# Performance work log

Hardware: AMD Instinct MI355X
Metric: run time of the kernel (lower is better)

The kernel has to match this reference:

```python
import jax, jax.numpy as jnp
import numpy as np

B, D, C, H = 65536, 256, 128, 1024
SPLIT = D // 2           # transformed half (odd indices under 'even' mask)
NET_IN = (D - SPLIT) + C # unchanged half + cond


def setup_inputs() -> dict:
    key = jax.random.key(0)
    ks = jax.random.split(key, 10)
    s = 0.02
    return {
        "x": jax.random.normal(ks[0], (B, D), jnp.float32),
        "cond": jax.random.normal(ks[1], (B, C), jnp.float32),
        "W1": jax.random.normal(ks[2], (NET_IN, H), jnp.float32) * s,
        "b1": jnp.zeros((H,), jnp.float32),
        "W2": jax.random.normal(ks[3], (H, H), jnp.float32) * s,
        "b2": jnp.zeros((H,), jnp.float32),
        "Ws": jax.random.normal(ks[4], (H, SPLIT), jnp.float32) * s,
        "bs": jnp.zeros((SPLIT,), jnp.float32),
        "Wt": jax.random.normal(ks[5], (H, SPLIT), jnp.float32) * s,
        "bt": jnp.zeros((SPLIT,), jnp.float32),
    }


def reference(x, cond, W1, b1, W2, b2, Ws, bs, Wt, bt):
    d = x.shape[1]
    even = jnp.arange(0, d, 2)  # mask==1 -> unchanged (x1)
    odd = jnp.arange(1, d, 2)   # mask==0 -> transformed (x2)
    x1u = x[:, even]            # (B, d - d//2)
    x2u = x[:, odd]             # (B, d//2)
    h = jax.nn.relu(jnp.concatenate([x1u, cond], axis=1) @ W1 + b1)
    h = jax.nn.relu(h @ W2 + b2)
    log_s = jnp.tanh(h @ Ws + bs)
    t = h @ Wt + bt
    x2t = x2u * jnp.exp(log_s) + t
    out = jnp.zeros_like(x).at[:, even].set(x1u).at[:, odd].set(x2t)
    log_det = jnp.sum(log_s, axis=1)
    return out, log_det
```

## Files before the change

### kernel.cpp

```cpp
#include <hip/hip_runtime.h>
#include <hip/hip_bf16.h>
#include <math.h>

#define B_ROWS 65536
#define D_DIM 256
#define C_DIM 128
#define H_DIM 1024

typedef __bf16 bf16x8 __attribute__((ext_vector_type(8)));
typedef float f32x4 __attribute__((ext_vector_type(4)));
typedef short short8 __attribute__((ext_vector_type(8)));

__device__ __forceinline__ unsigned short f2bf(float f) {
    unsigned int u = __float_as_uint(f);
    u += 0x7fffu + ((u >> 16) & 1u);
    return (unsigned short)(u >> 16);
}

__device__ __forceinline__ void gl2lds16(const void* g, void* l) {
    __builtin_amdgcn_global_load_lds(
        (const __attribute__((address_space(1))) unsigned int*)g,
        (__attribute__((address_space(3))) unsigned int*)l, 16, 0, 0);
}

__device__ __forceinline__ bf16x8 ds_read_b128_asm(const short* p) {
    bf16x8 r;
    asm volatile("ds_read_b128 %0, %1"
                 : "=v"(r)
                 : "v"((const __attribute__((address_space(3))) short*)p));
    return r;
}

__device__ __forceinline__ void swizzle_mn(int id, int mtiles, int& m, int& n) {
    if ((mtiles & 7) == 0) {
        int g = id >> 6, r = id & 63;
        m = g * 8 + (r & 7);
        n = r >> 3;
    } else {
        m = id >> 3;
        n = id & 7;
    }
}

__global__ void transpose_bf16(const float* __restrict__ src, short* __restrict__ dst,
                               int R, int C, int total) {
    int tid = blockIdx.x * 256 + threadIdx.x;
    if (tid >= total) return;
    int per = R >> 3;
    int n = tid / per;
    int k0 = (tid - n * per) << 3;
    short8 o;
#pragma unroll
    for (int j = 0; j < 8; ++j) o[j] = (short)f2bf(src[(size_t)(k0 + j) * C + n]);
    *(short8*)&dst[(size_t)n * R + k0] = o;
}

__global__ void prep_b3(const float* __restrict__ bs, const float* __restrict__ bt,
                        float* __restrict__ b3) {
    int i = threadIdx.x;
    b3[i] = (i < 128) ? bs[i] : bt[i - 128];
}

__global__ __launch_bounds__(256) void gemm1_fused(
    const float* __restrict__ x, const float* __restrict__ cond,
    const short* __restrict__ Bw, const float* __restrict__ bias,
    unsigned short* __restrict__ H1, int mtiles) {
    constexpr int BK = 64, K = 256, N = 1024;
    __shared__ __align__(16) short As[128 * BK];
    __shared__ __align__(16) short Bs[128 * BK];
    const int tid = threadIdx.x;
    const int lane = tid & 63;
    const int wave = tid >> 6;
    int mt, nt;
    swizzle_mn(blockIdx.x, mtiles, mt, nt);
    const int tm = mt * 128, tn = nt * 128;
    const int mo = (wave >> 1) * 64;
    const int no = (wave & 1) * 64;

    f32x4 acc[4][4];
#pragma unroll
    for (int i = 0; i < 4; ++i)
#pragma unroll
        for (int j = 0; j < 4; ++j) acc[i][j] = f32x4{0.f, 0.f, 0.f, 0.f};

    const int srow = lane >> 3;
    const int skb = (lane & 7) ^ srow;

#pragma unroll
    for (int kc = 0; kc < K; kc += BK) {
        __syncthreads();
#pragma unroll
        for (int i = 0; i < 4; ++i) {
            int c = wave * 4 + i;
            int row = c * 8 + srow;
            int kcol = kc + skb * 8;
            float v[8];
            if (kc < 128) {
                const float4* p = (const float4*)(x + (size_t)(tm + row) * 256 + 2 * kcol);
                float4 a = p[0], b = p[1], cc = p[2], d = p[3];
                v[0]=a.x; v[1]=a.z; v[2]=b.x; v[3]=b.z; v[4]=cc.x; v[5]=cc.z; v[6]=d.x; v[7]=d.z;
            } else {
                const float4* p = (const float4*)(cond + (size_t)(tm + row) * 128 + (kcol - 128));
                float4 a = p[0], b = p[1];
                v[0]=a.x; v[1]=a.y; v[2]=a.z; v[3]=a.w; v[4]=b.x; v[5]=b.y; v[6]=b.z; v[7]=b.w;
            }
            short8 o;
#pragma unroll
            for (int j = 0; j < 8; ++j) o[j] = (short)f2bf(v[j]);
            *(short8*)&As[c * 512 + lane * 8] = o;
            gl2lds16(Bw + (size_t)(tn + row) * K + kc + skb * 8, &Bs[c * 512]);
        }
        __syncthreads();
#pragma unroll
        for (int kk = 0; kk < 2; ++kk) {
            bf16x8 af[4], bfr[4];
            int kb = kk * 4 + (lane >> 4);
#pragma unroll
            for (int t = 0; t < 4; ++t) {
                int r = mo + t * 16 + (lane & 15);
                af[t] = *(const bf16x8*)&As[r * BK + ((kb ^ (r & 7)) << 3)];
                int n = no + t * 16 + (lane & 15);
                bfr[t] = *(const bf16x8*)&Bs[n * BK + ((kb ^ (n & 7)) << 3)];
            }
#pragma unroll
            for (int i = 0; i < 4; ++i)
#pragma unroll
                for (int j = 0; j < 4; ++j)
                    acc[i][j] = __builtin_amdgcn_mfma_f32_16x16x32_bf16(
                        af[i], bfr[j], acc[i][j], 0, 0, 0);
        }
    }

#pragma unroll
    for (int j = 0; j < 4; ++j) {
        int col = tn + no + j * 16 + (lane & 15);
        float bb = bias[col];
#pragma unroll
        for (int i = 0; i < 4; ++i) {
            int row0 = tm + mo + i * 16 + ((lane >> 4) << 2);
            f32x4 v = acc[i][j];
#pragma unroll
            for (int rr = 0; rr < 4; ++rr)
                H1[(size_t)(row0 + rr) * N + col] = f2bf(fmaxf(v[rr] + bb, 0.f));
        }
    }
}

__global__ __launch_bounds__(256) void gemm_tn(
    const short* __restrict__ A, const short* __restrict__ Bw,
    const float* __restrict__ bias, unsigned short* __restrict__ Cout,
    int mtiles, int N, int K) {
    constexpr int BK = 64;
    __shared__ __align__(16) short As[128 * BK];
    __shared__ __align__(16) short Bs[128 * BK];
    const int tid = threadIdx.x;
    const int lane = tid & 63;
    const int wave = tid >> 6;
    int mt, nt;
    swizzle_mn(blockIdx.x, mtiles, mt, nt);
    const int tm = mt * 128, tn = nt * 128;
    const int mo = (wave >> 1) * 64;
    const int no = (wave & 1) * 64;

    f32x4 acc[4][4];
#pragma unroll
    for (int i = 0; i < 4; ++i)
#pragma unroll
        for (int j = 0; j < 4; ++j) acc[i][j] = f32x4{0.f, 0.f, 0.f, 0.f};

    const int srow = lane >> 3;
    const int skb = (lane & 7) ^ srow;

    for (int kc = 0; kc < K; kc += BK) {
        __syncthreads();
#pragma unroll
        for (int i = 0; i < 4; ++i) {
            int c = wave * 4 + i;
            int row = c * 8 + srow;
            gl2lds16(A + (size_t)(tm + row) * K + kc + skb * 8, &As[c * 512]);
            gl2lds16(Bw + (size_t)(tn + row) * K + kc + skb * 8, &Bs[c * 512]);
        }
        __syncthreads();
#pragma unroll
        for (int kk = 0; kk < 2; ++kk) {
            bf16x8 af[4], bfr[4];
            int kb = kk * 4 + (lane >> 4);
#pragma unroll
            for (int t = 0; t < 4; ++t) {
                int r = mo + t * 16 + (lane & 15);
                af[t] = *(const bf16x8*)&As[r * BK + ((kb ^ (r & 7)) << 3)];
                int n = no + t * 16 + (lane & 15);
                bfr[t] = *(const bf16x8*)&Bs[n * BK + ((kb ^ (n & 7)) << 3)];
            }
#pragma unroll
            for (int i = 0; i < 4; ++i)
#pragma unroll
                for (int j = 0; j < 4; ++j)
                    acc[i][j] = __builtin_amdgcn_mfma_f32_16x16x32_bf16(
                        af[i], bfr[j], acc[i][j], 0, 0, 0);
        }
    }

#pragma unroll
    for (int j = 0; j < 4; ++j) {
        int col = tn + no + j * 16 + (lane & 15);
        float bb = bias[col];
#pragma unroll
        for (int i = 0; i < 4; ++i) {
            int row0 = tm + mo + i * 16 + ((lane >> 4) << 2);
            f32x4 v = acc[i][j];
#pragma unroll
            for (int rr = 0; rr < 4; ++rr)
                Cout[(size_t)(row0 + rr) * N + col] = f2bf(fmaxf(v[rr] + bb, 0.f));
        }
    }
}

__global__ __launch_bounds__(512, 2) void gemm2_8ph(
    const short* __restrict__ A, const short* __restrict__ Bw,
    const float* __restrict__ bias, unsigned short* __restrict__ Cout) {
    constexpr int K = 1024, NT = 16;
    constexpr unsigned OFF_A0 = 0, OFF_B0 = 16384, OFF_A1 = 32768, OFF_B1 = 49152;
    __shared__ __align__(16) short smem[65536];

    const int tid = threadIdx.x;
    const int lane = tid & 63;
    const int wave = tid >> 6;
    const int wm = wave >> 2;
    const int wn = wave & 3;
    const int l15 = lane & 15;
    const int quad = lane >> 4;
    const int srow = lane >> 3;
    const int skb8 = ((lane & 7) ^ srow) << 3;

    const int id = blockIdx.x, nwg = gridDim.x;
    const int xcd = id & 7, lid = id >> 3;
    const int q = nwg >> 3, r = nwg & 7;
    const int wgid = (xcd < r ? xcd * (q + 1) : r * (q + 1) + (xcd - r) * q) + lid;
    const int mt = wgid >> 2, nt = wgid & 3;
    const size_t Abase = (size_t)(mt * 256) * K;
    const size_t Bbase = (size_t)(nt * 256) * K;

    f32x4 acc[8][4];
#pragma unroll
    for (int m = 0; m < 8; ++m)
#pragma unroll
        for (int n = 0; n < 4; ++n) acc[m][n] = f32x4{0.f, 0.f, 0.f, 0.f};

    auto stage2 = [&](unsigned off, const short* g, size_t rowbase, int kc, int c0, int c1) {
        gl2lds16(g + rowbase + (size_t)(c0 * 8 + srow) * K + kc + skb8, smem + off + c0 * 512);
        gl2lds16(g + rowbase + (size_t)(c1 * 8 + srow) * K + kc + skb8, smem + off + c1 * 512);
    };
    auto stageU = [&](int u, unsigned aOff, unsigned bOff, int kc) {
        if (u == 0)      stage2(bOff, Bw, Bbase, kc, wave * 2, wave * 2 + 1);
        else if (u == 1) stage2(bOff, Bw, Bbase, kc, 16 + wave * 2, 17 + wave * 2);
        else if (u == 2) stage2(aOff, A, Abase, kc, wave, 16 + wave);
        else             stage2(aOff, A, Abase, kc, 8 + wave, 24 + wave);
    };

    const unsigned x0 = (unsigned)((quad ^ (l15 & 7)) << 3);
    const unsigned x1 = (unsigned)(((4 + quad) ^ (l15 & 7)) << 3);

    auto window = [&](int w, unsigned caOff, unsigned cbOff, unsigned naOff, unsigned nbOff) {
        const int kc1 = (w + 1) << 6, kc2 = (w + 2) << 6;
        const short* aA = smem + caOff + ((wm << 7) + l15) * 64;
        const short* aB = smem + cbOff + ((wn << 6) + l15) * 64;
        bf16x8 bfr[4][2], af[2][2];

#pragma unroll
        for (int n = 0; n < 4; ++n) {
            bfr[n][0] = ds_read_b128_asm(aB + n * 1024 + x0);
            bfr[n][1] = ds_read_b128_asm(aB + n * 1024 + x1);
        }
#pragma unroll
        for (int mm = 0; mm < 2; ++mm) {
            af[mm][0] = ds_read_b128_asm(aA + mm * 1024 + x0);
            af[mm][1] = ds_read_b128_asm(aA + mm * 1024 + x1);
        }
        if (w + 1 < NT) stageU(3, naOff, nbOff, kc1);
        __builtin_amdgcn_sched_barrier(0);
        __builtin_amdgcn_s_barrier();
        asm volatile("s_waitcnt lgkmcnt(0)" ::: "memory");
        __builtin_amdgcn_sched_barrier(0);
        __builtin_amdgcn_s_setprio(1);
#pragma unroll
        for (int kk = 0; kk < 2; ++kk)
#pragma unroll
            for (int mm = 0; mm < 2; ++mm)
#pragma unroll
                for (int n = 0; n < 4; ++n)
                    acc[mm][n] = __builtin_amdgcn_mfma_f32_16x16x32_bf16(
                        af[mm][kk], bfr[n][kk], acc[mm][n], 0, 0, 0);
        __builtin_amdgcn_s_setprio(0);

#pragma unroll
        for (int ph = 1; ph < 4; ++ph) {
#pragma unroll
            for (int mm = 0; mm < 2; ++mm) {
                af[mm][0] = ds_read_b128_asm(aA + (ph * 2 + mm) * 1024 + x0);
                af[mm][1] = ds_read_b128_asm(aA + (ph * 2 + mm) * 1024 + x1);
            }
            if (w + 2 < NT) stageU(ph - 1, caOff, cbOff, kc2);
            if (ph == 3) {
                if (w < NT - 2)
                    asm volatile("s_waitcnt vmcnt(6)" ::: "memory");
                else
                    asm volatile("s_waitcnt vmcnt(0)" ::: "memory");
            }
            __builtin_amdgcn_sched_barrier(0);
            __builtin_amdgcn_s_barrier();
            asm volatile("s_waitcnt lgkmcnt(0)" ::: "memory");
            __builtin_amdgcn_sched_barrier(0);
            __builtin_amdgcn_s_setprio(1);
#pragma unroll
            for (int kk = 0; kk < 2; ++kk)
#pragma unroll
                for (int mm = 0; mm < 2; ++mm)
#pragma unroll
                    for (int n = 0; n < 4; ++n)
                        acc[ph * 2 + mm][n] = __builtin_amdgcn_mfma_f32_16x16x32_bf16(
                            af[mm][kk], bfr[n][kk], acc[ph * 2 + mm][n], 0, 0, 0);
            __builtin_amdgcn_s_setprio(0);
        }
    };

    stageU(0, OFF_A0, OFF_B0, 0);
    stageU(1, OFF_A0, OFF_B0, 0);
    stageU(2, OFF_A0, OFF_B0, 0);
    stageU(3, OFF_A0, OFF_B0, 0);
    stageU(0, OFF_A1, OFF_B1, 64);
    stageU(1, OFF_A1, OFF_B1, 64);
    stageU(2, OFF_A1, OFF_B1, 64);
    asm volatile("s_waitcnt vmcnt(6)" ::: "memory");
    __builtin_amdgcn_sched_barrier(0);
    __builtin_amdgcn_s_barrier();

#pragma unroll 1
    for (int w = 0; w < NT; w += 2) {
        window(w, OFF_A0, OFF_B0, OFF_A1, OFF_B1);
        window(w + 1, OFF_A1, OFF_B1, OFF_A0, OFF_B0);
    }

    __syncthreads();
    unsigned short* cs = (unsigned short*)smem;
#pragma unroll
    for (int n = 0; n < 4; ++n) {
        int colblk = wn * 4 + n;
        int col = (colblk << 4) + l15;
        float bb = bias[nt * 256 + col];
#pragma unroll
        for (int m = 0; m < 8; ++m) {
            int row = (wm << 7) + m * 16 + (quad << 2);
#pragma unroll
            for (int rr = 0; rr < 4; ++rr) {
                int rw = row + rr;
                int sb = colblk ^ ((rw >> 2) & 3);
                cs[rw * 256 + (sb << 4) + l15] = f2bf(fmaxf(acc[m][n][rr] + bb, 0.f));
            }
        }
    }
    __syncthreads();
    const size_t cbase = (size_t)(mt * 256) * 1024 + nt * 256;
    const int rloc = tid >> 5, cchunk = tid & 31;
#pragma unroll
    for (int rnd = 0; rnd < 16; ++rnd) {
        int rw = rnd * 16 + rloc;
        int blk = cchunk >> 1, half = cchunk & 1;
        int sb = blk ^ ((rw >> 2) & 3);
        short8 v = *(const short8*)&cs[rw * 256 + (sb << 4) + half * 8];
        *(short8*)((unsigned short*)Cout + cbase + (size_t)rw * 1024 + cchunk * 8) = v;
    }
}

__global__ __launch_bounds__(256) void gemm3_final(
    const short* __restrict__ H2, const short* __restrict__ W3T,
    const float* __restrict__ b3, const float* __restrict__ x,
    float* __restrict__ out, float* __restrict__ logdet) {
    constexpr int BK = 64, K = 1024;
    __shared__ __align__(16) char raw[40960];
    __shared__ float rowsum[64];
    short* As = (short*)raw;
    short* Bs = (short*)(raw + 8192);
    float* Tbuf = (float*)raw;
    const int tid = threadIdx.x;
    const int lane = tid & 63;
    const int wave = tid >> 6;
    const int tm = blockIdx.x * 64;
    const int srow = lane >> 3;
    const int skb = (lane & 7) ^ srow;
    const int l15 = lane & 15;
    const int quad = lane >> 4;

    if (tid < 64) rowsum[tid] = 0.f;

    f32x4 acc[4][4];
#pragma unroll
    for (int i = 0; i < 4; ++i)
#pragma unroll
        for (int j = 0; j < 4; ++j) acc[i][j] = f32x4{0.f, 0.f, 0.f, 0.f};

    for (int kc = 0; kc < K; kc += BK) {
        __syncthreads();
#pragma unroll
        for (int i = 0; i < 10; ++i) {
            int c = wave * 10 + i;
            if (c < 8) {
                int row = c * 8 + srow;
                gl2lds16(H2 + (size_t)(tm + row) * K + kc + skb * 8, &As[c * 512]);
            } else {
                int row = (c - 8) * 8 + srow;
                gl2lds16(W3T + (size_t)row * K + kc + skb * 8, &Bs[(c - 8) * 512]);
            }
        }
        __syncthreads();
#pragma unroll
        for (int kk = 0; kk < 2; ++kk) {
            int kb = kk * 4 + quad;
            bf16x8 af[4], bfr[4];
#pragma unroll
            for (int mt = 0; mt < 4; ++mt) {
                int r = mt * 16 + l15;
                af[mt] = *(const bf16x8*)&As[r * BK + ((kb ^ (r & 7)) << 3)];
            }
#pragma unroll
            for (int nt = 0; nt < 4; ++nt) {
                int n = wave * 64 + nt * 16 + l15;
                bfr[nt] = *(const bf16x8*)&Bs[n * BK + ((kb ^ (n & 7)) << 3)];
            }
#pragma unroll
            for (int mt = 0; mt < 4; ++mt)
#pragma unroll
                for (int nt = 0; nt < 4; ++nt)
                    acc[mt][nt] = __builtin_amdgcn_mfma_f32_16x16x32_bf16(
                        af[mt], bfr[nt], acc[mt][nt], 0, 0, 0);
        }
    }

    __syncthreads();
    if (wave >= 2) {
#pragma unroll
        for (int nt = 0; nt < 4; ++nt) {
            int col = wave * 64 + nt * 16 + l15;
            float bb = b3[col];
            int cl = col - 128;
#pragma unroll
            for (int mt = 0; mt < 4; ++mt) {
#pragma unroll
                for (int rr = 0; rr < 4; ++rr) {
                    int m = mt * 16 + quad * 4 + rr;
                    Tbuf[m * 132 + cl] = acc[mt][nt][rr] + bb;
                }
            }
        }
    }
    __syncthreads();
    if (wave < 2) {
#pragma unroll
        for (int mt = 0; mt < 4; ++mt) {
#pragma unroll
            for (int rr = 0; rr < 4; ++rr) {
                int m = mt * 16 + quad * 4 + rr;
                int grow = tm + m;
                float s = 0.f;
#pragma unroll
                for (int nt = 0; nt < 4; ++nt) {
                    int j = wave * 64 + nt * 16 + l15;
                    float p = acc[mt][nt][rr] + b3[j];
                    p = fminf(fmaxf(p, -15.f), 15.f);
                    float e2 = __expf(2.f * p);
                    float ls = (e2 - 1.f) / (e2 + 1.f);
                    s += ls;
                    float tt = Tbuf[m * 132 + j];
                    float2 xv = *(const float2*)&x[(size_t)grow * 256 + 2 * j];
                    float2 ov;
                    ov.x = xv.x;
                    ov.y = xv.y * __expf(ls) + tt;
                    *(float2*)&out[(size_t)grow * 256 + 2 * j] = ov;
                }
                s += __shfl_xor(s, 1);
                s += __shfl_xor(s, 2);
                s += __shfl_xor(s, 4);
                s += __shfl_xor(s, 8);
                if (l15 == 0) atomicAdd(&rowsum[m], s);
            }
        }
    }
    __syncthreads();
    if (tid < 64) logdet[tm + tid] = rowsum[tid];
}

extern "C" void kernel_launch(void* const* d_in, const int* in_sizes, int n_in,
                              void* d_out, int out_size, void* d_ws, size_t ws_size,
                              hipStream_t stream) {
    const float* x = (const float*)d_in[0];
    const float* cond = (const float*)d_in[1];
    const float* W1 = (const float*)d_in[2];
    const float* b1 = (const float*)d_in[3];
    const float* W2 = (const float*)d_in[4];
    const float* b2 = (const float*)d_in[5];
    const float* Wsp = (const float*)d_in[6];
    const float* bs = (const float*)d_in[7];
    const float* Wtp = (const float*)d_in[8];
    const float* bt = (const float*)d_in[9];

    char* ws = (char*)d_ws;
    short* W1T = (short*)(ws);
    short* W2T = (short*)(ws + 524288ull);
    short* W3T = (short*)(ws + 2621440ull);
    float* b3  = (float*)(ws + 3145728ull);
    const size_t chunk_base = 3149824ull;

    int n_chunks = 1;
    while (n_chunks < 512) {
        size_t rp = (size_t)B_ROWS / n_chunks;
        if (chunk_base + rp * 4096ull <= ws_size) break;
        n_chunks *= 2;
    }
    const size_t RP = (size_t)B_ROWS / n_chunks;

    float* out = (float*)d_out;
    float* logdet = out + (size_t)B_ROWS * D_DIM;

    transpose_bf16<<<(32768 + 255) / 256, 256, 0, stream>>>(W1, W1T, 256, 1024, 32768);
    transpose_bf16<<<(131072 + 255) / 256, 256, 0, stream>>>(W2, W2T, 1024, 1024, 131072);
    transpose_bf16<<<(16384 + 255) / 256, 256, 0, stream>>>(Wsp, W3T, 1024, 128, 16384);
    transpose_bf16<<<(16384 + 255) / 256, 256, 0, stream>>>(Wtp, W3T + 131072, 1024, 128, 16384);
    prep_b3<<<1, 256, 0, stream>>>(bs, bt, b3);

    for (int c = 0; c < n_chunks; ++c) {
        const size_t r0 = (size_t)c * RP;
        short* H1 = (short*)(ws + chunk_base);
        short* H2 = (short*)(ws + chunk_base + 2048ull * RP);
        const int mtiles = (int)(RP / 128);

        gemm1_fused<<<mtiles * 8, 256, 0, stream>>>(
            x + r0 * D_DIM, cond + r0 * C_DIM, W1T, b1, (unsigned short*)H1, mtiles);
        if ((RP & 255) == 0) {
            gemm2_8ph<<<(int)(RP / 256) * 4, 512, 0, stream>>>(
                H1, W2T, b2, (unsigned short*)H2);
        } else {
            gemm_tn<<<mtiles * 8, 256, 0, stream>>>(
                H1, W2T, b2, (unsigned short*)H2, mtiles, H_DIM, H_DIM);
        }
        gemm3_final<<<(int)(RP / 64), 256, 0, stream>>>(
            H2, W3T, b3, x + r0 * D_DIM, out + r0 * D_DIM, logdet + r0);
    }
}
```

Baseline: 471.4 us.

## Pre-convert first-layer inputs to bf16 and reuse pipelined GEMM for layer one

Adds a prep kernel that gathers the even columns of x and all of cond into a packed bf16 matrix in workspace. The first GEMM then runs on the templated 8-phase pipelined GEMM kernel (K=256) instead of the simple fused kernel that converted and gathered on the fly. This is meant to give layer one the better-pipelined MFMA path, at the cost of an extra full pass writing and reading a 32 MB intermediate and less workspace left for chunks.

```diff
diff --git a/kernel.cpp b/kernel.cpp
--- a/kernel.cpp
+++ b/kernel.cpp
@@ -61,89 +61,28 @@
     b3[i] = (i < 128) ? bs[i] : bt[i - 128];
 }
 
-__global__ __launch_bounds__(256) void gemm1_fused(
+__global__ __launch_bounds__(256) void prep_a(
     const float* __restrict__ x, const float* __restrict__ cond,
-    const short* __restrict__ Bw, const float* __restrict__ bias,
-    unsigned short* __restrict__ H1, int mtiles) {
-    constexpr int BK = 64, K = 256, N = 1024;
-    __shared__ __align__(16) short As[128 * BK];
-    __shared__ __align__(16) short Bs[128 * BK];
-    const int tid = threadIdx.x;
-    const int lane = tid & 63;
-    const int wave = tid >> 6;
-    int mt, nt;
-    swizzle_mn(blockIdx.x, mtiles, mt, nt);
-    const int tm = mt * 128, tn = nt * 128;
-    const int mo = (wave >> 1) * 64;
-    const int no = (wave & 1) * 64;
-
-    f32x4 acc[4][4];
-#pragma unroll
-    for (int i = 0; i < 4; ++i)
-#pragma unroll
-        for (int j = 0; j < 4; ++j) acc[i][j] = f32x4{0.f, 0.f, 0.f, 0.f};
-
-    const int srow = lane >> 3;
-    const int skb = (lane & 7) ^ srow;
-
-#pragma unroll
-    for (int kc = 0; kc < K; kc += BK) {
-        __syncthreads();
-#pragma unroll
-        for (int i = 0; i < 4; ++i) {
-            int c = wave * 4 + i;
-            int row = c * 8 + srow;
-            int kcol = kc + skb * 8;
-            float v[8];
-            if (kc < 128) {
-                const float4* p = (const float4*)(x + (size_t)(tm + row) * 256 + 2 * kcol);
-                float4 a = p[0], b = p[1], cc = p[2], d = p[3];
-                v[0]=a.x; v[1]=a.z; v[2]=b.x; v[3]=b.z; v[4]=cc.x; v[5]=cc.z; v[6]=d.x; v[7]=d.z;
-            } else {
-                const float4* p = (const float4*)(cond + (size_t)(tm + row) * 128 + (kcol - 128));
-                float4 a = p[0], b = p[1];
-                v[0]=a.x; v[1]=a.y; v[2]=a.z; v[3]=a.w; v[4]=b.x; v[5]=b.y; v[6]=b.z; v[7]=b.w;
-            }
-            short8 o;
-#pragma unroll
-            for (int j = 0; j < 8; ++j) o[j] = (short)f2bf(v[j]);
-            *(short8*)&As[c * 512 + lane * 8] = o;
-            gl2lds16(Bw + (size_t)(tn + row) * K + kc + skb * 8, &Bs[c * 512]);
-        }
-        __syncthreads();
-#pragma unroll
-        for (int kk = 0; kk < 2; ++kk) {
-            bf16x8 af[4], bfr[4];
-            int kb = kk * 4 + (lane >> 4);
-#pragma unroll
-            for (int t = 0; t < 4; ++t) {
-                int r = mo + t * 16 + (lane & 15);
-                af[t] = *(const bf16x8*)&As[r * BK + ((kb ^ (r & 7)) << 3)];
-                int n = no + t * 16 + (lane & 15);
-                bfr[t] = *(const bf16x8*)&Bs[n * BK + ((kb ^ (n & 7)) << 3)];
-            }
-#pragma unroll
-            for (int i = 0; i < 4; ++i)
-#pragma unroll
-                for (int j = 0; j < 4; ++j)
-                    acc[i][j] = __builtin_amdgcn_mfma_f32_16x16x32_bf16(
-                        af[i], bfr[j], acc[i][j], 0, 0, 0);
-        }
-    }
-
-#pragma unroll
-    for (int j = 0; j < 4; ++j) {
-        int col = tn + no + j * 16 + (lane & 15);
-        float bb = bias[col];
-#pragma unroll
-        for (int i = 0; i < 4; ++i) {
-            int row0 = tm + mo + i * 16 + ((lane >> 4) << 2);
-            f32x4 v = acc[i][j];
-#pragma unroll
-            for (int rr = 0; rr < 4; ++rr)
-                H1[(size_t)(row0 + rr) * N + col] = f2bf(fmaxf(v[rr] + bb, 0.f));
-        }
-    }
+    short* __restrict__ A) {
+    int t = blockIdx.x * 256 + threadIdx.x;
+    int m = t >> 5, seg = t & 31;
+    short8 o;
+    if (seg < 16) {
+        const float4* p = (const float4*)(x + (size_t)m * 256 + seg * 16);
+        float4 a = p[0], b = p[1], c = p[2], d = p[3];
+        o[0] = (short)f2bf(a.x); o[1] = (short)f2bf(a.z);
+        o[2] = (short)f2bf(b.x); o[3] = (short)f2bf(b.z);
+        o[4] = (short)f2bf(c.x); o[5] = (short)f2bf(c.z);
+        o[6] = (short)f2bf(d.x); o[7] = (short)f2bf(d.z);
+    } else {
+        const float4* p = (const float4*)(cond + (size_t)m * 128 + (seg - 16) * 8);
+        float4 a = p[0], b = p[1];
+        o[0] = (short)f2bf(a.x); o[1] = (short)f2bf(a.y);
+        o[2] = (short)f2bf(a.z); o[3] = (short)f2bf(a.w);
+        o[4] = (short)f2bf(b.x); o[5] = (short)f2bf(b.y);
+        o[6] = (short)f2bf(b.z); o[7] = (short)f2bf(b.w);
+    }
+    *(short8*)&A[(size_t)m * 256 + seg * 8] = o;
 }
 
 __global__ __launch_bounds__(256) void gemm_tn(
@@ -216,10 +155,11 @@
     }
 }
 
+template<int K>
 __global__ __launch_bounds__(512, 2) void gemm2_8ph(
     const short* __restrict__ A, const short* __restrict__ Bw,
     const float* __restrict__ bias, unsigned short* __restrict__ Cout) {
-    constexpr int K = 1024, NT = 16;
+    constexpr int NT = K / 64;
     constexpr unsigned OFF_A0 = 0, OFF_B0 = 16384, OFF_A1 = 32768, OFF_B1 = 49152;
     __shared__ __align__(16) short smem[65536];
 
@@ -508,7 +448,8 @@
     short* W2T = (short*)(ws + 524288ull);
     short* W3T = (short*)(ws + 2621440ull);
     float* b3  = (float*)(ws + 3145728ull);
-    const size_t chunk_base = 3149824ull;
+    short* Aprep = (short*)(ws + 3149824ull);
+    const size_t chunk_base = 3149824ull + 33554432ull;
 
     int n_chunks = 1;
     while (n_chunks < 512) {
@@ -526,6 +467,7 @@
     transpose_bf16<<<(16384 + 255) / 256, 256, 0, stream>>>(Wsp, W3T, 1024, 128, 16384);
     transpose_bf16<<<(16384 + 255) / 256, 256, 0, stream>>>(Wtp, W3T + 131072, 1024, 128, 16384);
     prep_b3<<<1, 256, 0, stream>>>(bs, bt, b3);
+    prep_a<<<B_ROWS * 32 / 256, 256, 0, stream>>>(x, cond, Aprep);
 
     for (int c = 0; c < n_chunks; ++c) {
         const size_t r0 = (size_t)c * RP;
@@ -533,13 +475,15 @@
         short* H2 = (short*)(ws + chunk_base + 2048ull * RP);
         const int mtiles = (int)(RP / 128);
 
-        gemm1_fused<<<mtiles * 8, 256, 0, stream>>>(
-            x + r0 * D_DIM, cond + r0 * C_DIM, W1T, b1, (unsigned short*)H1, mtiles);
         if ((RP & 255) == 0) {
-            gemm2_8ph<<<(int)(RP / 256) * 4, 512, 0, stream>>>(
+            gemm2_8ph<256><<<(int)(RP / 256) * 4, 512, 0, stream>>>(
+                Aprep + r0 * 256, W1T, b1, (unsigned short*)H1);
+            gemm2_8ph<1024><<<(int)(RP / 256) * 4, 512, 0, stream>>>(
                 H1, W2T, b2, (unsigned short*)H2);
         } else {
             gemm_tn<<<mtiles * 8, 256, 0, stream>>>(
+                Aprep + r0 * 256, W1T, b1, (unsigned short*)H1, mtiles, H_DIM, 256);
+            gemm_tn<<<mtiles * 8, 256, 0, stream>>>(
                 H1, W2T, b2, (unsigned short*)H2, mtiles, H_DIM, H_DIM);
         }
         gemm3_final<<<(int)(RP / 64), 256, 0, stream>>>(
```

After: 460.1 us. -2.4%, faster.
